# Optimization experiments

Hardware: AMD Instinct MI355X
Metric: run time of the kernel (lower is better)

The kernel has to match this reference:

```python
import jax, jax.numpy as jnp
import numpy as np

B, F_DIM, H, W = 4, 256, 32, 32
DIM, DEPTH, HEADS, MLP_DIM = 768, 8, 12, 3072
DIM_HEAD = DIM // HEADS
SCALE = DIM_HEAD ** -0.5
LN_EPS = 1e-5


def sine_pos_embed(h, w, num_pos_feats):
    # PositionEmbeddingSine with normalize=True, scale=2*pi, temperature=10000
    scale = 2.0 * np.pi
    eps = 1e-6
    y = jnp.arange(1, h + 1, dtype=jnp.float32) / (h + eps) * scale  # [h]
    x = jnp.arange(1, w + 1, dtype=jnp.float32) / (w + eps) * scale  # [w]
    i = jnp.arange(num_pos_feats, dtype=jnp.float32)
    dim_t = 10000.0 ** (2.0 * jnp.floor(i / 2.0) / num_pos_feats)  # [F]

    def interleave(p):  # p: [..., F] -> sin of even dims, cos of odd dims, interleaved
        return jnp.stack([jnp.sin(p[..., 0::2]), jnp.cos(p[..., 1::2])], axis=-1).reshape(p.shape[:-1] + (-1,))

    pos_y = interleave(y[:, None] / dim_t)  # [h, F]
    pos_x = interleave(x[:, None] / dim_t)  # [w, F]
    pos = jnp.concatenate([
        jnp.broadcast_to(pos_y[:, None, :], (h, w, num_pos_feats)),
        jnp.broadcast_to(pos_x[None, :, :], (h, w, num_pos_feats)),
    ], axis=-1)  # [h, w, 2F]
    return pos.reshape(h * w, 2 * num_pos_feats)


def layer_norm(x, w, b):
    mu = jnp.mean(x, axis=-1, keepdims=True)
    var = jnp.var(x, axis=-1, keepdims=True)
    return (x - mu) * jax.lax.rsqrt(var + LN_EPS) * w + b


def setup_inputs() -> dict:
    key = jax.random.key(0)
    ks = jax.random.split(key, 16)
    s = lambda fan_in: 1.0 / np.sqrt(fan_in)
    return {
        "c_f": jax.random.normal(ks[0], (B, F_DIM, H, W), dtype=jnp.float32),
        "conv_w": jax.random.normal(ks[1], (DIM, F_DIM), dtype=jnp.float32) * s(F_DIM),
        "conv_b": jnp.zeros((DIM,), dtype=jnp.float32),
        "ln1_w": jnp.ones((DEPTH, DIM), dtype=jnp.float32),
        "ln1_b": jnp.zeros((DEPTH, DIM), dtype=jnp.float32),
        "qkv_w": jax.random.normal(ks[2], (DEPTH, DIM, 3 * DIM), dtype=jnp.float32) * s(DIM),
        "out_w": jax.random.normal(ks[3], (DEPTH, DIM, DIM), dtype=jnp.float32) * s(DIM),
        "out_b": jnp.zeros((DEPTH, DIM), dtype=jnp.float32),
        "ln2_w": jnp.ones((DEPTH, DIM), dtype=jnp.float32),
        "ln2_b": jnp.zeros((DEPTH, DIM), dtype=jnp.float32),
        "mlp_w1": jax.random.normal(ks[4], (DEPTH, DIM, MLP_DIM), dtype=jnp.float32) * s(DIM),
        "mlp_b1": jnp.zeros((DEPTH, MLP_DIM), dtype=jnp.float32),
        "mlp_w2": jax.random.normal(ks[5], (DEPTH, MLP_DIM, DIM), dtype=jnp.float32) * s(MLP_DIM),
        "mlp_b2": jnp.zeros((DEPTH, DIM), dtype=jnp.float32),
    }


def reference(c_f, conv_w, conv_b, ln1_w, ln1_b, qkv_w, out_w, out_b,
              ln2_w, ln2_b, mlp_w1, mlp_b1, mlp_w2, mlp_b2):
    b, _, h, w = c_f.shape
    n = h * w
    # 1x1 conv == per-pixel linear; tokens: [b, n, dim]
    x = jnp.einsum('bfn,df->bnd', c_f.reshape(b, F_DIM, n), conv_w) + conv_b
    x = x + sine_pos_embed(h, w, DIM // 2)[None]  # [b, n, dim]

    for l in range(DEPTH):
        # PreNorm multi-head self-attention + residual
        y = layer_norm(x, ln1_w[l], ln1_b[l])
        qkv = y @ qkv_w[l]  # [b, n, 3*dim]
        q, k, v = jnp.split(qkv, 3, axis=-1)
        to_heads = lambda t: t.reshape(b, n, HEADS, DIM_HEAD).transpose(0, 2, 1, 3)
        q, k, v = to_heads(q), to_heads(k), to_heads(v)
        dots = jnp.einsum('bhnd,bhmd->bhnm', q, k) * SCALE
        attn = jax.nn.softmax(dots, axis=-1)
        o = jnp.einsum('bhnm,bhmd->bhnd', attn, v)
        o = o.transpose(0, 2, 1, 3).reshape(b, n, DIM)
        x = o @ out_w[l] + out_b[l] + x
        # PreNorm MLP + residual
        y = layer_norm(x, ln2_w[l], ln2_b[l])
        hdd = jax.nn.gelu(y @ mlp_w1[l] + mlp_b1[l], approximate=False)
        x = hdd @ mlp_w2[l] + mlp_b2[l] + x

    return x.transpose(0, 2, 1).reshape(b, DIM, h, w)
```

## Files before the change

kernel.cpp:

```cpp
#include <hip/hip_runtime.h>
#include <stdint.h>

typedef unsigned short u16;
typedef __attribute__((ext_vector_type(8))) short short8;
typedef __attribute__((ext_vector_type(4))) short s16x4;
typedef __attribute__((ext_vector_type(4))) float f32x4;

struct P4 { float* p[4]; };

#define DEV __device__ __forceinline__

DEV u16 f2bf(float f) {
  union { float f; uint32_t u; } c; c.f = f;
  uint32_t u = c.u;
  uint32_t r = u + 0x7fffu + ((u >> 16) & 1u);
  return (u16)(r >> 16);
}

DEV void g2l16(const void* g, void* l) {
  __builtin_amdgcn_global_load_lds((__attribute__((address_space(1))) void*)(g),
                                   (__attribute__((address_space(3))) void*)(l),
                                   16, 0, 0);
}

__global__ void pos_kernel(float* __restrict__ pos) {
  int n = blockIdx.x;
  float yv = (float)((n >> 5) + 1) / (32.0f + 1e-6f) * 6.283185307179586f;
  float xv = (float)((n & 31) + 1) / (32.0f + 1e-6f) * 6.283185307179586f;
#pragma unroll
  for (int i = 0; i < 3; i++) {
    int d = threadIdx.x + i * 256;
    int dd = (d < 384) ? d : d - 384;
    float base = (d < 384) ? yv : xv;
    float ex = (float)(dd & ~1) / 384.0f;
    float arg = base / powf(10000.0f, ex);
    pos[(size_t)n * 768 + d] = (dd & 1) ? cosf(arg) : sinf(arg);
  }
}

__global__ void convw_kernel(const float* __restrict__ src, u16* __restrict__ dst) {
  int i = blockIdx.x * 256 + threadIdx.x;
  dst[i] = f2bf(src[i]);
}

DEV void tile_tr32(const float* __restrict__ src, u16* __restrict__ dst,
                   int R, int C, int tr, int tc, float (*tile)[33]) {
  int tx = threadIdx.x & 31, ty = threadIdx.x >> 5;
#pragma unroll
  for (int i = 0; i < 32; i += 8)
    tile[ty + i][tx] = src[(size_t)(tr * 32 + ty + i) * C + tc * 32 + tx];
  __syncthreads();
#pragma unroll
  for (int i = 0; i < 32; i += 8)
    dst[(size_t)(tc * 32 + ty + i) * R + tr * 32 + tx] = f2bf(tile[tx][ty + i]);
}

__global__ void wconv_kernel(const float* __restrict__ qkv_w, const float* __restrict__ out_w,
                             const float* __restrict__ m1w, const float* __restrict__ m2w,
                             u16* __restrict__ wqkv, u16* __restrict__ wout,
                             u16* __restrict__ wm1, u16* __restrict__ wm2, int layer) {
  __shared__ float tile[32][33];
  int tid = blockIdx.x;
  if (tid < 1728) {
    tile_tr32(qkv_w + (size_t)layer * 768 * 2304, wqkv, 768, 2304, tid / 72, tid % 72, tile);
  } else if (tid < 2304) {
    int t2 = tid - 1728;
    tile_tr32(out_w + (size_t)layer * 768 * 768, wout, 768, 768, t2 / 24, t2 % 24, tile);
  } else if (tid < 4608) {
    int t3 = tid - 2304;
    tile_tr32(m1w + (size_t)layer * 768 * 3072, wm1, 768, 3072, t3 / 96, t3 % 96, tile);
  } else {
    int t4 = tid - 4608;
    tile_tr32(m2w + (size_t)layer * 3072 * 768, wm2, 3072, 768, t4 / 24, t4 % 24, tile);
  }
}

__global__ void cf_tr_kernel(const float* __restrict__ c_f, u16* __restrict__ aconv) {
  __shared__ float tile[32][33];
  int b = blockIdx.z;
  tile_tr32(c_f + (size_t)b * 256 * 1024, aconv + (size_t)b * 1024 * 256,
            256, 1024, blockIdx.y, blockIdx.x, tile);
}

__global__ void out_tr_kernel(const float* __restrict__ x, float* __restrict__ out) {
  __shared__ float tile[32][33];
  int b = blockIdx.z;
  const float* src = x + (size_t)b * 1024 * 768;
  float* dst = out + (size_t)b * 768 * 1024;
  int tr = blockIdx.y, tc = blockIdx.x;
  int tx = threadIdx.x & 31, ty = threadIdx.x >> 5;
#pragma unroll
  for (int i = 0; i < 32; i += 8)
    tile[ty + i][tx] = src[(size_t)(tr * 32 + ty + i) * 768 + tc * 32 + tx];
  __syncthreads();
#pragma unroll
  for (int i = 0; i < 32; i += 8)
    dst[(size_t)(tc * 32 + ty + i) * 1024 + tr * 32 + tx] = tile[tx][ty + i];
}

__global__ __launch_bounds__(256) void ln_kernel(const float* __restrict__ x,
                                                 const float* __restrict__ w,
                                                 const float* __restrict__ bsh,
                                                 u16* __restrict__ y) {
  int row = blockIdx.x, t = threadIdx.x;
  const float* xr = x + (size_t)row * 768;
  float v[3], s = 0.f, sq = 0.f;
#pragma unroll
  for (int i = 0; i < 3; i++) { v[i] = xr[t + i * 256]; s += v[i]; sq += v[i] * v[i]; }
#pragma unroll
  for (int off = 32; off; off >>= 1) { s += __shfl_xor(s, off); sq += __shfl_xor(sq, off); }
  __shared__ float ss[4], ssq[4];
  if ((t & 63) == 0) { ss[t >> 6] = s; ssq[t >> 6] = sq; }
  __syncthreads();
  s = ss[0] + ss[1] + ss[2] + ss[3];
  sq = ssq[0] + ssq[1] + ssq[2] + ssq[3];
  float mean = s * (1.0f / 768.0f);
  float var = sq * (1.0f / 768.0f) - mean * mean;
  float rs = rsqrtf(var + 1e-5f);
#pragma unroll
  for (int i = 0; i < 3; i++) {
    int c = t + i * 256;
    y[(size_t)row * 768 + c] = f2bf((v[i] - mean) * rs * w[c] + bsh[c]);
  }
}

template <int S, bool DO_LN>
__global__ __launch_bounds__(256) void redln_kernel(P4 parts, const float* __restrict__ xin,
                                                    const float* __restrict__ bias,
                                                    const float* __restrict__ w,
                                                    const float* __restrict__ bsh,
                                                    float* __restrict__ xout,
                                                    u16* __restrict__ y) {
  int row = blockIdx.x, t = threadIdx.x;
  size_t base = (size_t)row * 768;
  float v[3], s = 0.f, sq = 0.f;
#pragma unroll
  for (int i = 0; i < 3; i++) {
    int c = t + i * 256;
    float acc = xin[base + c] + bias[c];
#pragma unroll
    for (int j = 0; j < S; j++) acc += parts.p[j][base + c];
    v[i] = acc;
    xout[base + c] = acc;
    s += acc; sq += acc * acc;
  }
  if constexpr (DO_LN) {
#pragma unroll
    for (int off = 32; off; off >>= 1) { s += __shfl_xor(s, off); sq += __shfl_xor(sq, off); }
    __shared__ float ss[4], ssq[4];
    if ((t & 63) == 0) { ss[t >> 6] = s; ssq[t >> 6] = sq; }
    __syncthreads();
    s = ss[0] + ss[1] + ss[2] + ss[3];
    sq = ssq[0] + ssq[1] + ssq[2] + ssq[3];
    float mean = s * (1.0f / 768.0f);
    float var = sq * (1.0f / 768.0f) - mean * mean;
    float rs = rsqrtf(var + 1e-5f);
#pragma unroll
    for (int i = 0; i < 3; i++) {
      int c = t + i * 256;
      y[base + c] = f2bf((v[i] - mean) * rs * w[c] + bsh[c]);
    }
  }
}

constexpr int EPI_BF16 = 0, EPI_BIAS_RES = 1, EPI_BIAS_GELU = 2, EPI_BIAS_POS = 3, EPI_PART = 4;

template <int EPI, int BN = 128>
__global__ __launch_bounds__(256, 2) void gemm_bt(
    const u16* __restrict__ A, const u16* __restrict__ BT,
    const float* __restrict__ bias, const float* __restrict__ res,
    void* __restrict__ Cout, int M, int N, int K, P4 parts) {
  constexpr int NF = BN / 32;
  __shared__ __align__(16) u16 As[128 * 32];
  __shared__ __align__(16) u16 Bs[BN * 32];
  const int t = threadIdx.x;
  const int w = t >> 6, l = t & 63, lr = l & 15, quad = l >> 4;
  const int bm = blockIdx.y * 128, bn = blockIdx.x * BN;
  const int wm = (w & 1) * 64, wn = (w >> 1) * (BN / 2);
  f32x4 acc[4][NF];
#pragma unroll
  for (int i = 0; i < 4; i++)
#pragma unroll
    for (int j = 0; j < NF; j++) acc[i][j] = (f32x4){0.f, 0.f, 0.f, 0.f};
  const int c0 = t, c1 = 256 + t;
  const size_t a0 = (size_t)(bm + (c0 >> 2)) * K + (c0 & 3) * 8;
  const size_t a1 = (size_t)(bm + (c1 >> 2)) * K + (c1 & 3) * 8;
  const size_t b0 = (size_t)(bn + (c0 >> 2)) * K + (c0 & 3) * 8;
  const size_t b1 = (BN == 128) ? (size_t)(bn + (c1 >> 2)) * K + (c1 & 3) * 8 : 0;
  const int kc = K / (int)gridDim.z;
  const int kBeg = (int)blockIdx.z * kc;
  for (int k0 = kBeg; k0 < kBeg + kc; k0 += 32) {
    g2l16(A + a0 + k0, As + c0 * 8);
    g2l16(A + a1 + k0, As + c1 * 8);
    g2l16(BT + b0 + k0, Bs + c0 * 8);
    if constexpr (BN == 128) g2l16(BT + b1 + k0, Bs + c1 * 8);
    __syncthreads();
    short8 af[4], bf[NF];
#pragma unroll
    for (int mi = 0; mi < 4; mi++) af[mi] = *(const short8*)(As + (wm + mi * 16 + lr) * 32 + quad * 8);
#pragma unroll
    for (int nj = 0; nj < NF; nj++) bf[nj] = *(const short8*)(Bs + (wn + nj * 16 + lr) * 32 + quad * 8);
#pragma unroll
    for (int mi = 0; mi < 4; mi++)
#pragma unroll
      for (int nj = 0; nj < NF; nj++)
        acc[mi][nj] = __builtin_amdgcn_mfma_f32_16x16x32_bf16(af[mi], bf[nj], acc[mi][nj], 0, 0, 0);
    __syncthreads();
  }
  float* Pc = (EPI == EPI_PART) ? parts.p[blockIdx.z] : nullptr;
#pragma unroll
  for (int mi = 0; mi < 4; mi++) {
    const int rowb = bm + wm + mi * 16 + quad * 4;
#pragma unroll
    for (int nj = 0; nj < NF; nj++) {
      const int gn = bn + wn + nj * 16 + lr;
#pragma unroll
      for (int r = 0; r < 4; r++) {
        const size_t idx = (size_t)(rowb + r) * N + gn;
        float v = acc[mi][nj][r];
        if constexpr (EPI == EPI_BF16) {
          ((u16*)Cout)[idx] = f2bf(v);
        } else if constexpr (EPI == EPI_BIAS_RES) {
          ((float*)Cout)[idx] = v + bias[gn] + res[idx];
        } else if constexpr (EPI == EPI_BIAS_GELU) {
          float xg = v + bias[gn];
          ((u16*)Cout)[idx] = f2bf(0.5f * xg * (1.0f + erff(xg * 0.70710678118f)));
        } else if constexpr (EPI == EPI_BIAS_POS) {
          ((float*)Cout)[idx] = v + bias[gn] + res[(size_t)((rowb + r) & 1023) * N + gn];
        } else {
          Pc[idx] = v;
        }
      }
    }
  }
}

__global__ __launch_bounds__(256) void vtr_kernel(const u16* __restrict__ qkvb,
                                                  u16* __restrict__ vT) {
  __shared__ uint32_t tile[64][65];
  const int t = threadIdx.x;
  const int bh = blockIdx.y, b = bh / 12, h = bh % 12;
  const int tok0 = blockIdx.x * 64;
  {
    int trow = t >> 2, dc = (t & 3) * 16;
    const u16* src = qkvb + (size_t)(b * 1024 + tok0 + trow) * 2304 + 1536 + h * 64 + dc;
    short8 v0 = *(const short8*)src;
    short8 v1 = *(const short8*)(src + 8);
#pragma unroll
    for (int j = 0; j < 8; j++) {
      tile[trow][dc + j] = (uint32_t)(u16)v0[j];
      tile[trow][dc + 8 + j] = (uint32_t)(u16)v1[j];
    }
  }
  __syncthreads();
  {
    int d = t >> 2, tc = (t & 3) * 16;
    short8 o0, o1;
#pragma unroll
    for (int j = 0; j < 8; j++) {
      o0[j] = (short)(u16)tile[tc + j][d];
      o1[j] = (short)(u16)tile[tc + 8 + j][d];
    }
    u16* dst = vT + (size_t)(bh * 64 + d) * 1024 + tok0 + tc;
    *(short8*)dst = o0;
    *(short8*)(dst + 8) = o1;
  }
}

__global__ __launch_bounds__(256, 3) void attn_kernel(const u16* __restrict__ qkv,
                                                      const u16* __restrict__ vT,
                                                      u16* __restrict__ o) {
  __shared__ __align__(16) u16 Ks[2][2 * 64 * 32];
  __shared__ __align__(16) u16 Vs[2][2 * 64 * 32];
  __shared__ __align__(16) u16 Ps[4][16 * 72];
  const int t = threadIdx.x;
  const int w = t >> 6, l = t & 63, lr = l & 15, quad = l >> 4;
  const int bh = blockIdx.y, b = bh / 12, h = bh % 12;
  const int qb = blockIdx.x * 64 + w * 16;
  const int swz = (lr >> 1) & 3;

  short8 aq[2];
#pragma unroll
  for (int ks = 0; ks < 2; ks++)
    aq[ks] = *(const short8*)(qkv + (size_t)(b * 1024 + qb + lr) * 2304 +
                              h * 64 + ks * 32 + quad * 8);

  const u16* kbase = qkv + (size_t)(b * 1024) * 2304 + 768 + h * 64;
  const u16* vbase = vT + (size_t)(bh * 64) * 1024;
  u16* Pw = Ps[w];

  f32x4 accO[4];
  float l_loc = 0.f;
#pragma unroll
  for (int dj = 0; dj < 4; dj++) accO[dj] = (f32x4){0.f, 0.f, 0.f, 0.f};

  auto stage = [&](int buf, int kb) {
#pragma unroll
    for (int pass = 0; pass < 2; pass++) {
      int u = pass * 256 + t;
      int ks = u >> 8, row = (u >> 2) & 63, c4 = u & 3;
      int cs = c4 ^ ((row >> 1) & 3);
      g2l16(kbase + (size_t)(kb + row) * 2304 + ks * 32 + cs * 8, Ks[buf] + (size_t)u * 8);
      g2l16(vbase + (size_t)row * 1024 + kb + ks * 32 + cs * 8, Vs[buf] + (size_t)u * 8);
    }
  };

  stage(0, 0);
  __syncthreads();
  int cur = 0;
  for (int kb = 0; kb < 1024; kb += 64) {
    if (kb + 64 < 1024) stage(cur ^ 1, kb + 64);

    f32x4 s[4];
#pragma unroll
    for (int nj = 0; nj < 4; nj++) s[nj] = (f32x4){0.f, 0.f, 0.f, 0.f};
#pragma unroll
    for (int ks = 0; ks < 2; ks++)
#pragma unroll
      for (int nj = 0; nj < 4; nj++) {
        short8 ak = *(const short8*)(Ks[cur] + ks * 2048 + (nj * 16 + lr) * 32 + (quad ^ swz) * 8);
        s[nj] = __builtin_amdgcn_mfma_f32_16x16x32_bf16(ak, aq[ks], s[nj], 0, 0, 0);
      }

    {
      const int rowoff = lr * 72;
#pragma unroll
      for (int nj = 0; nj < 4; nj++) {
        s16x4 pk;
#pragma unroll
        for (int r = 0; r < 4; r++) {
          float p = exp2f(s[nj][r] * 0.18033688011112042f);
          l_loc += p;
          pk[r] = (short)f2bf(p);
        }
        *(s16x4*)(Pw + rowoff + nj * 16 + quad * 4) = pk;
      }
    }

#pragma unroll
    for (int ks = 0; ks < 2; ks++) {
      short8 bp = *(const short8*)(Pw + lr * 72 + ks * 32 + quad * 8);
#pragma unroll
      for (int dj = 0; dj < 4; dj++) {
        short8 av = *(const short8*)(Vs[cur] + ks * 2048 + (dj * 16 + lr) * 32 + (quad ^ swz) * 8);
        accO[dj] = __builtin_amdgcn_mfma_f32_16x16x32_bf16(av, bp, accO[dj], 0, 0, 0);
      }
    }
    __syncthreads();
    cur ^= 1;
  }

  l_loc += __shfl_xor(l_loc, 16);
  l_loc += __shfl_xor(l_loc, 32);
  {
    float inv = 1.0f / l_loc;
    size_t grow = (size_t)(b * 1024 + qb + lr);
#pragma unroll
    for (int dj = 0; dj < 4; dj++) {
      s16x4 ov;
#pragma unroll
      for (int r = 0; r < 4; r++) ov[r] = (short)f2bf(accO[dj][r] * inv);
      *(s16x4*)(o + grow * 768 + h * 64 + dj * 16 + quad * 4) = ov;
    }
  }
}

extern "C" void kernel_launch(void* const* d_in, const int* in_sizes, int n_in,
                              void* d_out, int out_size, void* d_ws, size_t ws_size,
                              hipStream_t stream) {
  (void)in_sizes; (void)n_in; (void)out_size; (void)ws_size;
  const float* c_f    = (const float*)d_in[0];
  const float* conv_w = (const float*)d_in[1];
  const float* conv_b = (const float*)d_in[2];
  const float* ln1_w  = (const float*)d_in[3];
  const float* ln1_b  = (const float*)d_in[4];
  const float* qkv_w  = (const float*)d_in[5];
  const float* out_w  = (const float*)d_in[6];
  const float* out_b  = (const float*)d_in[7];
  const float* ln2_w  = (const float*)d_in[8];
  const float* ln2_b  = (const float*)d_in[9];
  const float* m1w    = (const float*)d_in[10];
  const float* m1b    = (const float*)d_in[11];
  const float* m2w    = (const float*)d_in[12];
  const float* m2b    = (const float*)d_in[13];
  float* out = (float*)d_out;

  const size_t PSZ = 4096ull * 768 * 4;

  char* p = (char*)d_ws;
  auto alloc = [&](size_t bytes) { char* q = p; p += (bytes + 255) & ~(size_t)255; return q; };
  float* x    = (float*)alloc(4096ull * 768 * 4);
  u16* y      = (u16*)alloc(4096ull * 768 * 2);
  u16* qkvb   = (u16*)alloc(4096ull * 2304 * 2);
  u16* ob     = (u16*)alloc(4096ull * 768 * 2);
  u16* hb     = (u16*)alloc(4096ull * 3072 * 2);
  u16* aconv  = (u16*)alloc(4096ull * 256 * 2);
  u16* convw  = (u16*)alloc(768ull * 256 * 2);
  u16* wqkv   = (u16*)alloc(2304ull * 768 * 2);
  u16* wout   = (u16*)alloc(768ull * 768 * 2);
  u16* wm1    = (u16*)alloc(3072ull * 768 * 2);
  float* pos  = (float*)alloc(1024ull * 768 * 4);
  u16* wm2    = (u16*)alloc(768ull * 3072 * 2);
  u16* vT = hb;

  P4 pm{};
  pm.p[0] = (float*)qkvb;
  pm.p[1] = (float*)((char*)qkvb + PSZ);
  pm.p[2] = (float*)out;
  pm.p[3] = (float*)aconv;
  P4 none{};

  pos_kernel<<<1024, 256, 0, stream>>>(pos);
  convw_kernel<<<768, 256, 0, stream>>>(conv_w, convw);
  cf_tr_kernel<<<dim3(32, 8, 4), 256, 0, stream>>>(c_f, aconv);
  gemm_bt<EPI_BIAS_POS, 64><<<dim3(12, 32), 256, 0, stream>>>(aconv, convw, conv_b, pos, x, 4096, 768, 256, none);

  for (int lyr = 0; lyr < 8; lyr++) {
    if (lyr == 0) {
      ln_kernel<<<4096, 256, 0, stream>>>(x, ln1_w, ln1_b, y);
    } else {
      redln_kernel<4, true><<<4096, 256, 0, stream>>>(pm, x, m2b + (lyr - 1) * 768,
                                                      ln1_w + lyr * 768, ln1_b + lyr * 768, x, y);
    }
    wconv_kernel<<<6912, 256, 0, stream>>>(qkv_w, out_w, m1w, m2w, wqkv, wout, wm1, wm2, lyr);
    gemm_bt<EPI_BF16><<<dim3(18, 32), 256, 0, stream>>>(y, wqkv, nullptr, nullptr, qkvb, 4096, 2304, 768, none);
    vtr_kernel<<<dim3(16, 48), 256, 0, stream>>>(qkvb, vT);
    attn_kernel<<<dim3(16, 48), 256, 0, stream>>>(qkvb, vT, ob);
    gemm_bt<EPI_BIAS_RES, 64><<<dim3(12, 32), 256, 0, stream>>>(ob, wout, out_b + lyr * 768, x, x, 4096, 768, 768, none);
    ln_kernel<<<4096, 256, 0, stream>>>(x, ln2_w + lyr * 768, ln2_b + lyr * 768, y);
    gemm_bt<EPI_BIAS_GELU><<<dim3(24, 32), 256, 0, stream>>>(y, wm1, m1b + lyr * 3072, nullptr, hb, 4096, 3072, 768, none);
    gemm_bt<EPI_PART><<<dim3(6, 32, 4), 256, 0, stream>>>(hb, wm2, nullptr, nullptr, nullptr, 4096, 768, 3072, pm);
  }
  redln_kernel<4, false><<<4096, 256, 0, stream>>>(pm, x, m2b + 7 * 768, nullptr, nullptr, x, nullptr);
  out_tr_kernel<<<dim3(24, 32, 4), 256, 0, stream>>>(x, out);
}
```

Before: 1.678 ms.

## Double-buffer GEMM LDS tiles and XOR-swizzle K chunks to cut bank conflicts

The bf16 GEMM now keeps two LDS buffers for the A and B tiles and prefetches the next K-slice with direct global-to-LDS loads while MFMAs run on the current slice. This removes one barrier per iteration and hides global load latency. It also XOR-swizzles the 8-element chunk position within each 32-wide row, so fragment reads from LDS spread across banks. LDS use doubles per block, which may limit occupancy under the 2-blocks-per-CU launch bound. Correctness depends on the swizzle applied to the global source offset matching the swizzle applied to the read index.

```diff
diff --git a/kernel.cpp b/kernel.cpp
--- a/kernel.cpp
+++ b/kernel.cpp
@@ -171,41 +171,54 @@
     const float* __restrict__ bias, const float* __restrict__ res,
     void* __restrict__ Cout, int M, int N, int K, P4 parts) {
   constexpr int NF = BN / 32;
-  __shared__ __align__(16) u16 As[128 * 32];
-  __shared__ __align__(16) u16 Bs[BN * 32];
+  __shared__ __align__(16) u16 As[2][128 * 32];
+  __shared__ __align__(16) u16 Bs[2][BN * 32];
   const int t = threadIdx.x;
   const int w = t >> 6, l = t & 63, lr = l & 15, quad = l >> 4;
   const int bm = blockIdx.y * 128, bn = blockIdx.x * BN;
   const int wm = (w & 1) * 64, wn = (w >> 1) * (BN / 2);
+  const int swz = (lr >> 1) & 3;
   f32x4 acc[4][NF];
 #pragma unroll
   for (int i = 0; i < 4; i++)
 #pragma unroll
     for (int j = 0; j < NF; j++) acc[i][j] = (f32x4){0.f, 0.f, 0.f, 0.f};
   const int c0 = t, c1 = 256 + t;
-  const size_t a0 = (size_t)(bm + (c0 >> 2)) * K + (c0 & 3) * 8;
-  const size_t a1 = (size_t)(bm + (c1 >> 2)) * K + (c1 & 3) * 8;
-  const size_t b0 = (size_t)(bn + (c0 >> 2)) * K + (c0 & 3) * 8;
-  const size_t b1 = (BN == 128) ? (size_t)(bn + (c1 >> 2)) * K + (c1 & 3) * 8 : 0;
+  const int s0 = (c0 & 3) ^ ((c0 >> 3) & 3);
+  const int s1 = (c1 & 3) ^ ((c1 >> 3) & 3);
+  const size_t a0 = (size_t)(bm + (c0 >> 2)) * K + s0 * 8;
+  const size_t a1 = (size_t)(bm + (c1 >> 2)) * K + s1 * 8;
+  const size_t b0 = (size_t)(bn + (c0 >> 2)) * K + s0 * 8;
+  const size_t b1 = (BN == 128) ? (size_t)(bn + (c1 >> 2)) * K + s1 * 8 : 0;
   const int kc = K / (int)gridDim.z;
   const int kBeg = (int)blockIdx.z * kc;
+
+  auto stage = [&](int buf, int k0) {
+    g2l16(A + a0 + k0, As[buf] + c0 * 8);
+    g2l16(A + a1 + k0, As[buf] + c1 * 8);
+    g2l16(BT + b0 + k0, Bs[buf] + c0 * 8);
+    if constexpr (BN == 128) g2l16(BT + b1 + k0, Bs[buf] + c1 * 8);
+  };
+
+  stage(0, kBeg);
+  __syncthreads();
+  int cur = 0;
   for (int k0 = kBeg; k0 < kBeg + kc; k0 += 32) {
-    g2l16(A + a0 + k0, As + c0 * 8);
-    g2l16(A + a1 + k0, As + c1 * 8);
-    g2l16(BT + b0 + k0, Bs + c0 * 8);
-    if constexpr (BN == 128) g2l16(BT + b1 + k0, Bs + c1 * 8);
-    __syncthreads();
+    if (k0 + 32 < kBeg + kc) stage(cur ^ 1, k0 + 32);
     short8 af[4], bf[NF];
 #pragma unroll
-    for (int mi = 0; mi < 4; mi++) af[mi] = *(const short8*)(As + (wm + mi * 16 + lr) * 32 + quad * 8);
-#pragma unroll
-    for (int nj = 0; nj < NF; nj++) bf[nj] = *(const short8*)(Bs + (wn + nj * 16 + lr) * 32 + quad * 8);
+    for (int mi = 0; mi < 4; mi++)
+      af[mi] = *(const short8*)(As[cur] + (wm + mi * 16 + lr) * 32 + (quad ^ swz) * 8);
+#pragma unroll
+    for (int nj = 0; nj < NF; nj++)
+      bf[nj] = *(const short8*)(Bs[cur] + (wn + nj * 16 + lr) * 32 + (quad ^ swz) * 8);
 #pragma unroll
     for (int mi = 0; mi < 4; mi++)
 #pragma unroll
       for (int nj = 0; nj < NF; nj++)
         acc[mi][nj] = __builtin_amdgcn_mfma_f32_16x16x32_bf16(af[mi], bf[nj], acc[mi][nj], 0, 0, 0);
     __syncthreads();
+    cur ^= 1;
   }
   float* Pc = (EPI == EPI_PART) ? parts.p[blockIdx.z] : nullptr;
 #pragma unroll
```

New measurement: 1.670 ms. About the same (-0.5%).
